# Performance work log

Hardware: AMD Instinct MI355X
Metric: run time of the kernel (lower is better)

Reference implementation:

```python
import jax, jax.numpy as jnp
import numpy as np

A = -0.75  # torch bicubic kernel parameter

def _cubic_weights(t):
    # torch get_cubic_upsample_coefficients, a = -0.75; t = frac in [0, 1)
    def k1(x):  # |x| <= 1
        return ((A + 2.0) * x - (A + 3.0)) * x * x + 1.0
    def k2(x):  # 1 < |x| < 2
        return ((A * x - 5.0 * A) * x + 8.0 * A) * x - 4.0 * A
    return (k2(t + 1.0), k1(t), k1(1.0 - t), k2(2.0 - t))

def _reflect_clip(idx, size):
    # reflection padding about border pixel centers (align_corners=True), then clip
    span = size - 1
    i = jnp.abs(idx)
    i = jnp.mod(i, 2 * span)
    i = jnp.where(i > span, 2 * span - i, i)
    return jnp.clip(i, 0, span)

def _grid_sample_bicubic(img, gx, gy):
    # img: (C,H,W); gx,gy: (H,W) normalized coords (grid_sample convention)
    C, H, W = img.shape
    ix = (gx + 1.0) * 0.5 * (W - 1)  # align_corners=True unnormalize
    iy = (gy + 1.0) * 0.5 * (H - 1)
    x0 = jnp.floor(ix)
    y0 = jnp.floor(iy)
    wx = _cubic_weights(ix - x0)
    wy = _cubic_weights(iy - y0)
    x0i = x0.astype(jnp.int32)
    y0i = y0.astype(jnp.int32)
    out = jnp.zeros((C, H, W), img.dtype)
    for dy in range(4):
        yi = _reflect_clip(y0i + (dy - 1), H)
        row = jnp.zeros((C, H, W), img.dtype)
        for dx in range(4):
            xi = _reflect_clip(x0i + (dx - 1), W)
            row = row + wx[dx] * img[:, yi, xi]  # (C,H,W) gather
        out = out + wy[dy] * row
    return out

def setup_inputs() -> dict:
    key = jax.random.key(0)
    kx, kr, kc = jax.random.split(key, 3)
    B, C, H, W = 16, 8, 512, 512
    x = jax.random.normal(kx, (B, C, H, W), dtype=jnp.float32)
    rates = jnp.array([0.25, 0.5, 0.75], dtype=jnp.float32)
    idx = jax.random.randint(kr, (B,), 0, rates.shape[0])
    downsampling_rate = rates[idx]
    # center = 2*rand - 1, as in sample_downsampling_parameters
    center = 2.0 * jax.random.uniform(kc, (B, 2), dtype=jnp.float32) - 1.0
    return {"x": x, "downsampling_rate": downsampling_rate, "center": center}

def reference(x, downsampling_rate, center):
    B, C, H, W = x.shape
    # grid as built by get_downsampling_grid (module requires H == W)
    gx = (2.0 / W) * jnp.arange(W, dtype=x.dtype) - 1.0  # width coord  (channel 0)
    gy = (2.0 / H) * jnp.arange(H, dtype=x.dtype) - 1.0  # height coord (channel 1)
    gx = jnp.broadcast_to(gx[None, :], (H, W))
    gy = jnp.broadcast_to(gy[:, None], (H, W))
    r = downsampling_rate[:, None, None]                 # (B,1,1)
    cx = center[:, 0][:, None, None]
    cy = center[:, 1][:, None, None]
    Gx = (gx[None] - cx) / r + cx                        # (B,H,W)
    Gy = (gy[None] - cy) / r + cy
    return jax.vmap(_grid_sample_bicubic)(x, Gx, Gy)
```

## Files before the change

### kernel.cpp

```cpp
#include <hip/hip_runtime.h>

#define AA (-0.75f)

__device__ __forceinline__ float k1f(float x) {
    return ((AA + 2.0f) * x - (AA + 3.0f)) * x * x + 1.0f;
}
__device__ __forceinline__ float k2f(float x) {
    return ((AA * x - 5.0f * AA) * x + 8.0f * AA) * x - 4.0f * AA;
}

__device__ __forceinline__ int reflect_clip(int idx, int size) {
    int span = size - 1;
    int i = idx < 0 ? -idx : idx;
    i = i % (2 * span);
    if (i > span) i = 2 * span - i;
    return i;
}

__device__ __forceinline__ int swz(int a) { return a ^ ((a >> 5) & 31); }

__global__ __launch_bounds__(256)
void pds3_kernel(const float* __restrict__ x,
                 const float* __restrict__ rate,
                 const float* __restrict__ center,
                 float* __restrict__ out)
{
    constexpr int C = 8, H = 512, W = 512;

    const int orig = blockIdx.x;
    const int id = (orig & 7) * 1024 + (orig >> 3);
    const int b = id >> 9;
    const int h = id & (H - 1);

    const float r  = rate[b];
    const float cx = center[2 * b + 0];
    const float cy = center[2 * b + 1];

    const float gy = 0.00390625f * (float)h - 1.0f;
    const float Gy = (gy - cy) / r + cy;
    const float iy = (Gy + 1.0f) * 0.5f * 511.0f;
    const float y0 = floorf(iy);
    const float ty = iy - y0;
    const int   y0i = (int)y0;
    const float wy0 = k2f(ty + 1.0f);
    const float wy1 = k1f(ty);
    const float wy2 = k1f(1.0f - ty);
    const float wy3 = k2f(2.0f - ty);
    const size_t ro0 = (size_t)reflect_clip(y0i - 1, H) * W;
    const size_t ro1 = (size_t)reflect_clip(y0i    , H) * W;
    const size_t ro2 = (size_t)reflect_clip(y0i + 1, H) * W;
    const size_t ro3 = (size_t)reflect_clip(y0i + 2, H) * W;

    const int t = threadIdx.x;
    int   sA0, sA1, sA2, sA3, sB0, sB1, sB2, sB3;
    float wxA0, wxA1, wxA2, wxA3, wxB0, wxB1, wxB2, wxB3;
    {
        const int w = 2 * t;
        const float gx = 0.00390625f * (float)w - 1.0f;
        const float Gx = (gx - cx) / r + cx;
        const float ix = (Gx + 1.0f) * 0.5f * 511.0f;
        const float x0 = floorf(ix);
        const float tx = ix - x0;
        const int x0i = (int)x0;
        wxA0 = k2f(tx + 1.0f); wxA1 = k1f(tx);
        wxA2 = k1f(1.0f - tx); wxA3 = k2f(2.0f - tx);
        sA0 = swz(reflect_clip(x0i - 1, W)); sA1 = swz(reflect_clip(x0i,     W));
        sA2 = swz(reflect_clip(x0i + 1, W)); sA3 = swz(reflect_clip(x0i + 2, W));
    }
    {
        const int w = 2 * t + 1;
        const float gx = 0.00390625f * (float)w - 1.0f;
        const float Gx = (gx - cx) / r + cx;
        const float ix = (Gx + 1.0f) * 0.5f * 511.0f;
        const float x0 = floorf(ix);
        const float tx = ix - x0;
        const int x0i = (int)x0;
        wxB0 = k2f(tx + 1.0f); wxB1 = k1f(tx);
        wxB2 = k1f(1.0f - tx); wxB3 = k2f(2.0f - tx);
        sB0 = swz(reflect_clip(x0i - 1, W)); sB1 = swz(reflect_clip(x0i,     W));
        sB2 = swz(reflect_clip(x0i + 1, W)); sB3 = swz(reflect_clip(x0i + 2, W));
    }

    __shared__ float tmp[C][W];

    const float* imgb = x + (size_t)b * C * H * W;
    #pragma unroll
    for (int k = 0; k < 4; ++k) {
        const int g  = t + k * 256;
        const int c  = g >> 7;
        const int c4 = (g & 127) << 2;
        const float* img = imgb + (size_t)c * (H * W);
        const float4 a0 = *(const float4*)(img + ro0 + c4);
        const float4 a1 = *(const float4*)(img + ro1 + c4);
        const float4 a2 = *(const float4*)(img + ro2 + c4);
        const float4 a3 = *(const float4*)(img + ro3 + c4);
        float e0 = wy0 * a0.x + wy1 * a1.x + wy2 * a2.x + wy3 * a3.x;
        float e1 = wy0 * a0.y + wy1 * a1.y + wy2 * a2.y + wy3 * a3.y;
        float e2 = wy0 * a0.z + wy1 * a1.z + wy2 * a2.z + wy3 * a3.z;
        float e3 = wy0 * a0.w + wy1 * a1.w + wy2 * a2.w + wy3 * a3.w;
        const int v    = (c4 >> 5) & 31;
        const int base = c4 ^ (v & ~3);
        const int p    = v & 3;
        const bool q1 = (p & 1) != 0;
        const bool q2 = (p & 2) != 0;
        float t0 = q1 ? e1 : e0;
        float t1 = q1 ? e0 : e1;
        float t2 = q1 ? e3 : e2;
        float t3 = q1 ? e2 : e3;
        float u0 = q2 ? t2 : t0;
        float u1 = q2 ? t3 : t1;
        float u2 = q2 ? t0 : t2;
        float u3 = q2 ? t1 : t3;
        *(float4*)&tmp[c][base] = make_float4(u0, u1, u2, u3);
    }
    __syncthreads();

    float* obase = out + ((size_t)b * C * H + h) * W + 2 * t;
    #pragma unroll
    for (int c = 0; c < C; ++c) {
        const float* tr = tmp[c];
        const float s0 = wxA0 * tr[sA0] + wxA1 * tr[sA1]
                       + wxA2 * tr[sA2] + wxA3 * tr[sA3];
        const float s1 = wxB0 * tr[sB0] + wxB1 * tr[sB1]
                       + wxB2 * tr[sB2] + wxB3 * tr[sB3];
        *(float2*)(obase + (size_t)c * (H * W)) = make_float2(s0, s1);
    }
}

extern "C" void kernel_launch(void* const* d_in, const int* in_sizes, int n_in,
                              void* d_out, int out_size, void* d_ws, size_t ws_size,
                              hipStream_t stream) {
    const float* x      = (const float*)d_in[0];
    const float* rate   = (const float*)d_in[1];
    const float* center = (const float*)d_in[2];
    float* out          = (float*)d_out;

    constexpr int B = 16, H = 512;
    dim3 grid(B * H);
    dim3 block(256);
    pds3_kernel<<<grid, block, 0, stream>>>(x, rate, center, out);
}
```

Before: 61.14 us.

## Process four output rows per block with double-buffered software-pipelined row loads

```diff
diff --git a/kernel.cpp b/kernel.cpp
--- a/kernel.cpp
+++ b/kernel.cpp
@@ -1,4 +1,5 @@
 #include <hip/hip_runtime.h>
+#include <string.h>
 
 #define AA (-0.75f)
 
@@ -19,39 +20,24 @@
 
 __device__ __forceinline__ int swz(int a) { return a ^ ((a >> 5) & 31); }
 
-__global__ __launch_bounds__(256)
-void pds3_kernel(const float* __restrict__ x,
+__global__ __launch_bounds__(256, 4)
+void pds4_kernel(const float* __restrict__ x,
                  const float* __restrict__ rate,
                  const float* __restrict__ center,
                  float* __restrict__ out)
 {
-    constexpr int C = 8, H = 512, W = 512;
+    constexpr int C = 8, H = 512, W = 512, ROWS = 4;
 
     const int orig = blockIdx.x;
-    const int id = (orig & 7) * 1024 + (orig >> 3);
-    const int b = id >> 9;
-    const int h = id & (H - 1);
+    const int id = (orig & 7) * 256 + (orig >> 3);
+    const int b  = id >> 7;
+    const int h0 = (id & 127) * ROWS;
 
     const float r  = rate[b];
     const float cx = center[2 * b + 0];
     const float cy = center[2 * b + 1];
+    const int t = threadIdx.x;
 
-    const float gy = 0.00390625f * (float)h - 1.0f;
-    const float Gy = (gy - cy) / r + cy;
-    const float iy = (Gy + 1.0f) * 0.5f * 511.0f;
-    const float y0 = floorf(iy);
-    const float ty = iy - y0;
-    const int   y0i = (int)y0;
-    const float wy0 = k2f(ty + 1.0f);
-    const float wy1 = k1f(ty);
-    const float wy2 = k1f(1.0f - ty);
-    const float wy3 = k2f(2.0f - ty);
-    const size_t ro0 = (size_t)reflect_clip(y0i - 1, H) * W;
-    const size_t ro1 = (size_t)reflect_clip(y0i    , H) * W;
-    const size_t ro2 = (size_t)reflect_clip(y0i + 1, H) * W;
-    const size_t ro3 = (size_t)reflect_clip(y0i + 2, H) * W;
-
-    const int t = threadIdx.x;
     int   sA0, sA1, sA2, sA3, sB0, sB1, sB2, sB3;
     float wxA0, wxA1, wxA2, wxA3, wxB0, wxB1, wxB2, wxB3;
     {
@@ -81,50 +67,116 @@
         sB2 = swz(reflect_clip(x0i + 1, W)); sB3 = swz(reflect_clip(x0i + 2, W));
     }
 
-    __shared__ float tmp[C][W];
+    __shared__ float buf[2][C][W];
 
     const float* imgb = x + (size_t)b * C * H * W;
+
+    int cch[4], cc4[4];
     #pragma unroll
     for (int k = 0; k < 4; ++k) {
-        const int g  = t + k * 256;
-        const int c  = g >> 7;
-        const int c4 = (g & 127) << 2;
-        const float* img = imgb + (size_t)c * (H * W);
-        const float4 a0 = *(const float4*)(img + ro0 + c4);
-        const float4 a1 = *(const float4*)(img + ro1 + c4);
-        const float4 a2 = *(const float4*)(img + ro2 + c4);
-        const float4 a3 = *(const float4*)(img + ro3 + c4);
-        float e0 = wy0 * a0.x + wy1 * a1.x + wy2 * a2.x + wy3 * a3.x;
-        float e1 = wy0 * a0.y + wy1 * a1.y + wy2 * a2.y + wy3 * a3.y;
-        float e2 = wy0 * a0.z + wy1 * a1.z + wy2 * a2.z + wy3 * a3.z;
-        float e3 = wy0 * a0.w + wy1 * a1.w + wy2 * a2.w + wy3 * a3.w;
-        const int v    = (c4 >> 5) & 31;
-        const int base = c4 ^ (v & ~3);
-        const int p    = v & 3;
-        const bool q1 = (p & 1) != 0;
-        const bool q2 = (p & 2) != 0;
-        float t0 = q1 ? e1 : e0;
-        float t1 = q1 ? e0 : e1;
-        float t2 = q1 ? e3 : e2;
-        float t3 = q1 ? e2 : e3;
-        float u0 = q2 ? t2 : t0;
-        float u1 = q2 ? t3 : t1;
-        float u2 = q2 ? t0 : t2;
-        float u3 = q2 ? t1 : t3;
-        *(float4*)&tmp[c][base] = make_float4(u0, u1, u2, u3);
+        const int g = t + k * 256;
+        cch[k] = g >> 7;
+        cc4[k] = (g & 127) << 2;
+    }
+
+    float4 pf[4][4];
+    float  wyN0, wyN1, wyN2, wyN3;
+
+#define YTAPS(hh, w0, w1, w2, w3, r0, r1, r2, r3)                         \
+    {                                                                      \
+        const float gy = 0.00390625f * (float)(hh) - 1.0f;                 \
+        const float Gy = (gy - cy) / r + cy;                               \
+        const float iy = (Gy + 1.0f) * 0.5f * 511.0f;                      \
+        const float y0 = floorf(iy);                                       \
+        const float ty = iy - y0;                                          \
+        const int   y0i = (int)y0;                                         \
+        w0 = k2f(ty + 1.0f); w1 = k1f(ty);                                 \
+        w2 = k1f(1.0f - ty); w3 = k2f(2.0f - ty);                          \
+        r0 = (size_t)reflect_clip(y0i - 1, H) * W;                         \
+        r1 = (size_t)reflect_clip(y0i    , H) * W;                         \
+        r2 = (size_t)reflect_clip(y0i + 1, H) * W;                         \
+        r3 = (size_t)reflect_clip(y0i + 2, H) * W;                         \
+    }
+
+#define ISSUE(r0, r1, r2, r3)                                              \
+    _Pragma("unroll")                                                      \
+    for (int k = 0; k < 4; ++k) {                                          \
+        const float* img = imgb + (size_t)cch[k] * (H * W);                \
+        pf[k][0] = *(const float4*)(img + (r0) + cc4[k]);                  \
+        pf[k][1] = *(const float4*)(img + (r1) + cc4[k]);                  \
+        pf[k][2] = *(const float4*)(img + (r2) + cc4[k]);                  \
+        pf[k][3] = *(const float4*)(img + (r3) + cc4[k]);                  \
+    }
+
+#define COMBINE(dstbuf, w0, w1, w2, w3)                                    \
+    _Pragma("unroll")                                                      \
+    for (int k = 0; k < 4; ++k) {                                          \
+        const float4 a0 = pf[k][0], a1 = pf[k][1],                         \
+                     a2 = pf[k][2], a3 = pf[k][3];                         \
+        float e0 = w0 * a0.x + w1 * a1.x + w2 * a2.x + w3 * a3.x;          \
+        float e1 = w0 * a0.y + w1 * a1.y + w2 * a2.y + w3 * a3.y;          \
+        float e2 = w0 * a0.z + w1 * a1.z + w2 * a2.z + w3 * a3.z;          \
+        float e3 = w0 * a0.w + w1 * a1.w + w2 * a2.w + w3 * a3.w;          \
+        const int c4   = cc4[k];                                           \
+        const int v    = (c4 >> 5) & 31;                                   \
+        const int base = c4 ^ (v & ~3);                                    \
+        const int p    = v & 3;                                            \
+        const bool q1 = (p & 1) != 0;                                      \
+        const bool q2 = (p & 2) != 0;                                      \
+        float t0 = q1 ? e1 : e0;                                           \
+        float t1 = q1 ? e0 : e1;                                           \
+        float t2 = q1 ? e3 : e2;                                           \
+        float t3 = q1 ? e2 : e3;                                           \
+        float u0 = q2 ? t2 : t0;                                           \
+        float u1 = q2 ? t3 : t1;                                           \
+        float u2 = q2 ? t0 : t2;                                           \
+        float u3 = q2 ? t1 : t3;                                           \
+        *(float4*)&(dstbuf)[cch[k]][base] = make_float4(u0, u1, u2, u3);   \
+    }
+
+    {
+        size_t ro0, ro1, ro2, ro3;
+        YTAPS(h0, wyN0, wyN1, wyN2, wyN3, ro0, ro1, ro2, ro3);
+        ISSUE(ro0, ro1, ro2, ro3);
+        COMBINE(buf[0], wyN0, wyN1, wyN2, wyN3);
     }
     __syncthreads();
 
-    float* obase = out + ((size_t)b * C * H + h) * W + 2 * t;
     #pragma unroll
-    for (int c = 0; c < C; ++c) {
-        const float* tr = tmp[c];
-        const float s0 = wxA0 * tr[sA0] + wxA1 * tr[sA1]
-                       + wxA2 * tr[sA2] + wxA3 * tr[sA3];
-        const float s1 = wxB0 * tr[sB0] + wxB1 * tr[sB1]
-                       + wxB2 * tr[sB2] + wxB3 * tr[sB3];
-        *(float2*)(obase + (size_t)c * (H * W)) = make_float2(s0, s1);
+    for (int j = 0; j < ROWS; ++j) {
+        const int h = h0 + j;
+
+        if (j < ROWS - 1) {
+            size_t ro0, ro1, ro2, ro3;
+            YTAPS(h + 1, wyN0, wyN1, wyN2, wyN3, ro0, ro1, ro2, ro3);
+            ISSUE(ro0, ro1, ro2, ro3);
+        }
+
+        {
+            const float* trow0 = &buf[j & 1][0][0];
+            float* obase = out + ((size_t)b * C * H + h) * W + 2 * t;
+            #pragma unroll
+            for (int c = 0; c < C; ++c) {
+                const float* tr = trow0 + c * W;
+                const float s0 = wxA0 * tr[sA0] + wxA1 * tr[sA1]
+                               + wxA2 * tr[sA2] + wxA3 * tr[sA3];
+                const float s1 = wxB0 * tr[sB0] + wxB1 * tr[sB1]
+                               + wxB2 * tr[sB2] + wxB3 * tr[sB3];
+                float2 v2 = make_float2(s0, s1);
+                double dv;
+                memcpy(&dv, &v2, 8);
+                __builtin_nontemporal_store(dv, (double*)(obase + (size_t)c * (H * W)));
+            }
+        }
+
+        if (j < ROWS - 1) {
+            COMBINE(buf[(j + 1) & 1], wyN0, wyN1, wyN2, wyN3);
+            __syncthreads();
+        }
     }
+#undef YTAPS
+#undef ISSUE
+#undef COMBINE
 }
 
 extern "C" void kernel_launch(void* const* d_in, const int* in_sizes, int n_in,
@@ -135,8 +187,8 @@
     const float* center = (const float*)d_in[2];
     float* out          = (float*)d_out;
 
-    constexpr int B = 16, H = 512;
-    dim3 grid(B * H);
+    constexpr int B = 16, H = 512, ROWS = 4;
+    dim3 grid(B * (H / ROWS));
     dim3 block(256);
-    pds3_kernel<<<grid, block, 0, stream>>>(x, rate, center, out);
+    pds4_kernel<<<grid, block, 0, stream>>>(x, rate, center, out);
 }
```

New measurement: 85.14 us. +39.2%, slower.
